# Kernel optimization log

Measured on AMD Instinct MI355X. Metric: run time of the kernel, lower is better.

The kernel has to match this reference:

```python
import jax, jax.numpy as jnp
import numpy as np
from jax import lax

VOCAB, EMB, HID, NCLS, BATCH, SEQ = 32000, 512, 512, 8, 64, 512


def setup_inputs() -> dict:
    key = jax.random.key(0)
    ks = jax.random.split(key, 12)
    s = 0.05
    return {
        "x": jax.random.randint(ks[0], (BATCH, SEQ), 0, VOCAB),
        "emb": jax.random.normal(ks[1], (VOCAB, EMB), jnp.float32) * s,
        "W_ih0": jax.random.normal(ks[2], (HID, EMB), jnp.float32) * s,
        "W_hh0": jax.random.normal(ks[3], (HID, HID), jnp.float32) * s,
        "b_ih0": jax.random.normal(ks[4], (HID,), jnp.float32) * s,
        "b_hh0": jax.random.normal(ks[5], (HID,), jnp.float32) * s,
        "W_ih1": jax.random.normal(ks[6], (HID, HID), jnp.float32) * s,
        "W_hh1": jax.random.normal(ks[7], (HID, HID), jnp.float32) * s,
        "b_ih1": jax.random.normal(ks[8], (HID,), jnp.float32) * s,
        "b_hh1": jax.random.normal(ks[9], (HID,), jnp.float32) * s,
        "fc_W": jax.random.normal(ks[10], (NCLS, HID), jnp.float32) * s,
        "fc_b": jax.random.normal(ks[11], (NCLS,), jnp.float32) * s,
    }


def _rnn_layer(inp, W_ih, W_hh, b_ih, b_hh):
    # inp: [B, S, F]; tanh RNN, batch_first. Precompute input projection once.
    pre = jnp.einsum('bsf,hf->bsh', inp, W_ih) + b_ih + b_hh  # [B,S,H]
    B = inp.shape[0]
    H = W_hh.shape[0]
    h0 = jnp.zeros((B, H), inp.dtype)

    def step(h, p_t):  # p_t: [B,H]
        h = jnp.tanh(p_t + h @ W_hh.T)
        return h, h

    hT, ys = lax.scan(step, h0, pre.transpose(1, 0, 2))  # scan over time
    return ys.transpose(1, 0, 2), hT  # outputs [B,S,H], last hidden [B,H]


def reference(x, emb, W_ih0, W_hh0, b_ih0, b_hh0, W_ih1, W_hh1, b_ih1, b_hh1, fc_W, fc_b):
    xe = emb[x]  # [B,S,E] embedding lookup
    out0, _ = _rnn_layer(xe, W_ih0, W_hh0, b_ih0, b_hh0)
    _, h1 = _rnn_layer(out0, W_ih1, W_hh1, b_ih1, b_hh1)  # hidden[-1]
    return h1 @ fc_W.T + fc_b  # [B, n_class]
```

## Files before the change

kernel.cpp:

```cpp
#include <hip/hip_runtime.h>
#include <stdint.h>


#define BB 64
#define SS 512
#define HH 512

typedef short bf16x8 __attribute__((ext_vector_type(8)));
typedef float f32x4 __attribute__((ext_vector_type(4)));
typedef int i32x4 __attribute__((ext_vector_type(4)));
typedef unsigned int u32;
typedef u32 u32x2 __attribute__((ext_vector_type(2)));

__device__ __forceinline__ unsigned short f2bf(float f) {
  uint32_t u = __builtin_bit_cast(uint32_t, f);
  u += 0x7FFFu + ((u >> 16) & 1u);
  return (unsigned short)(u >> 16);
}
__device__ __forceinline__ float bf2f(unsigned short h) {
  uint32_t u = ((uint32_t)h) << 16;
  return __builtin_bit_cast(float, u);
}
__device__ __forceinline__ int pack2(unsigned short a, unsigned short b) {
  return (int)(unsigned int)a | ((int)(unsigned int)b << 16);
}
__device__ __forceinline__ u32 hipack(u32 a, u32 b) {
  return (a >> 16) | (b & 0xFFFF0000u);
}
__device__ __forceinline__ u32 lopack(u32 a, u32 b) {
  return (a & 0xFFF8u) | ((b & 0xFFF8u) << 16);
}
__device__ __forceinline__ bool tag4(i32x4 v, u32 t) {
  u32 m = (((u32)v[0] ^ t) | ((u32)v[1] ^ t) | ((u32)v[2] ^ t) | ((u32)v[3] ^ t)) & 7u;
  return m == 0u;
}
__device__ __forceinline__ float fast_tanh(float v) {
  float a = __builtin_fabsf(v);
  float e = __expf(-2.0f * a);
  float t = (1.0f - e) / (1.0f + e);
  return __builtin_copysignf(t, v);
}

#define UC_LOAD4(dst, ptr) \
  asm volatile("global_load_dwordx4 %0, %1, off sc0 sc1" : "=v"(dst) : "v"(ptr))
#define UC_LOAD1(dst, ptr) \
  asm volatile("global_load_dword %0, %1, off sc0 sc1" : "=v"(dst) : "v"(ptr))
#define UC_STORE2(ptr, v) \
  asm volatile("global_store_dwordx2 %0, %1, off sc0 sc1" ::"v"(ptr), "v"(v) : "memory")

#define ISSUE8(a0, a1, a2, a3, a4, a5, a6, a7, base)  \
  do {                                                \
    UC_LOAD4(a0, (base) + 8 * gch + 0);               \
    UC_LOAD4(a1, (base) + 8 * gch + 4);               \
    UC_LOAD4(a2, (base) + 8 * gch + 128);             \
    UC_LOAD4(a3, (base) + 8 * gch + 132);             \
    UC_LOAD4(a4, (base) + 8 * gch + 256);             \
    UC_LOAD4(a5, (base) + 8 * gch + 260);             \
    UC_LOAD4(a6, (base) + 8 * gch + 384);             \
    UC_LOAD4(a7, (base) + 8 * gch + 388);             \
  } while (0)

#define TAGOK8(a0, a1, a2, a3, a4, a5, a6, a7, t)                         \
  (tag4(a0, t) && tag4(a1, t) && tag4(a2, t) && tag4(a3, t) &&            \
   tag4(a4, t) && tag4(a5, t) && tag4(a6, t) && tag4(a7, t))

#define STAGE_IN0(w0, w1, w2, w3, w4, w5, w6, w7)                          \
  do {                                                                     \
    i32x4 A;                                                               \
    A[0] = (int)hipack(w0[0], w0[1]); A[1] = (int)hipack(w0[2], w0[3]);    \
    A[2] = (int)hipack(w1[0], w1[1]); A[3] = (int)hipack(w1[2], w1[3]);    \
    *(i32x4*)(s_in0 + gr * 512 + (((gch + 0) ^ (gr & 7)) << 3)) = A;       \
    A[0] = (int)hipack(w2[0], w2[1]); A[1] = (int)hipack(w2[2], w2[3]);    \
    A[2] = (int)hipack(w3[0], w3[1]); A[3] = (int)hipack(w3[2], w3[3]);    \
    *(i32x4*)(s_in0 + gr * 512 + (((gch + 16) ^ (gr & 7)) << 3)) = A;      \
    A[0] = (int)hipack(w4[0], w4[1]); A[1] = (int)hipack(w4[2], w4[3]);    \
    A[2] = (int)hipack(w5[0], w5[1]); A[3] = (int)hipack(w5[2], w5[3]);    \
    *(i32x4*)(s_in0 + gr * 512 + (((gch + 32) ^ (gr & 7)) << 3)) = A;      \
    A[0] = (int)hipack(w6[0], w6[1]); A[1] = (int)hipack(w6[2], w6[3]);    \
    A[2] = (int)hipack(w7[0], w7[1]); A[3] = (int)hipack(w7[2], w7[3]);    \
    *(i32x4*)(s_in0 + gr * 512 + (((gch + 48) ^ (gr & 7)) << 3)) = A;      \
  } while (0)

#define STAGE_H(w0, w1, w2, w3, w4, w5, w6, w7)                            \
  do {                                                                     \
    i32x4 A, B;                                                            \
    A[0] = (int)hipack(w0[0], w0[1]); A[1] = (int)hipack(w0[2], w0[3]);    \
    A[2] = (int)hipack(w1[0], w1[1]); A[3] = (int)hipack(w1[2], w1[3]);    \
    B[0] = (int)lopack(w0[0], w0[1]); B[1] = (int)lopack(w0[2], w0[3]);    \
    B[2] = (int)lopack(w1[0], w1[1]); B[3] = (int)lopack(w1[2], w1[3]);    \
    *(i32x4*)(s_Hhi + gr * 512 + (((gch + 0) ^ (gr & 7)) << 3)) = A;       \
    *(i32x4*)(s_Hlo + gr * 512 + (((gch + 0) ^ (gr & 7)) << 3)) = B;       \
    A[0] = (int)hipack(w2[0], w2[1]); A[1] = (int)hipack(w2[2], w2[3]);    \
    A[2] = (int)hipack(w3[0], w3[1]); A[3] = (int)hipack(w3[2], w3[3]);    \
    B[0] = (int)lopack(w2[0], w2[1]); B[1] = (int)lopack(w2[2], w2[3]);    \
    B[2] = (int)lopack(w3[0], w3[1]); B[3] = (int)lopack(w3[2], w3[3]);    \
    *(i32x4*)(s_Hhi + gr * 512 + (((gch + 16) ^ (gr & 7)) << 3)) = A;      \
    *(i32x4*)(s_Hlo + gr * 512 + (((gch + 16) ^ (gr & 7)) << 3)) = B;      \
    A[0] = (int)hipack(w4[0], w4[1]); A[1] = (int)hipack(w4[2], w4[3]);    \
    A[2] = (int)hipack(w5[0], w5[1]); A[3] = (int)hipack(w5[2], w5[3]);    \
    B[0] = (int)lopack(w4[0], w4[1]); B[1] = (int)lopack(w4[2], w4[3]);    \
    B[2] = (int)lopack(w5[0], w5[1]); B[3] = (int)lopack(w5[2], w5[3]);    \
    *(i32x4*)(s_Hhi + gr * 512 + (((gch + 32) ^ (gr & 7)) << 3)) = A;      \
    *(i32x4*)(s_Hlo + gr * 512 + (((gch + 32) ^ (gr & 7)) << 3)) = B;      \
    A[0] = (int)hipack(w6[0], w6[1]); A[1] = (int)hipack(w6[2], w6[3]);    \
    A[2] = (int)hipack(w7[0], w7[1]); A[3] = (int)hipack(w7[2], w7[3]);    \
    B[0] = (int)lopack(w6[0], w6[1]); B[1] = (int)lopack(w6[2], w6[3]);    \
    B[2] = (int)lopack(w7[0], w7[1]); B[3] = (int)lopack(w7[2], w7[3]);    \
    *(i32x4*)(s_Hhi + gr * 512 + (((gch + 48) ^ (gr & 7)) << 3)) = A;      \
    *(i32x4*)(s_Hlo + gr * 512 + (((gch + 48) ^ (gr & 7)) << 3)) = B;      \
  } while (0)

__global__ __launch_bounds__(512, 1) void k_rnn(
    const int* __restrict__ x, const float* __restrict__ emb,
    const float* __restrict__ Wih0, const float* __restrict__ Whh0,
    const float* __restrict__ bih0, const float* __restrict__ bhh0,
    const float* __restrict__ Wih1, const float* __restrict__ Whh1,
    const float* __restrict__ bih1, const float* __restrict__ bhh1,
    u32* __restrict__ hsl) {
  const int tid = threadIdx.x;
  const int bid = blockIdx.x;
  const int layer = bid >> 5;
  const int lb = bid & 31;
  const int bg = lb >> 3;
  const int c = lb & 7;
  const int wid = tid >> 6;
  const int lane = tid & 63;
  const int kq = wid >> 1;
  const int nh = wid & 1;
  const int gt = tid & 255;
  const int gr = gt >> 4;
  const int gch = gt & 15;
  const int s_row = (wid & 3) * 4 + ((lane & 31) >> 3);
  const int s_pub = lane & 7;

  __shared__ __align__(16) unsigned short s_in0[16 * 512];
  __shared__ __align__(16) unsigned short s_Hhi[16 * 512];
  __shared__ __align__(16) unsigned short s_Hlo[16 * 512];
  __shared__ __align__(16) float s_part[4 * 16 * 64];

  const float* Wih = layer ? Wih1 : Wih0;
  const float* Whh = layer ? Whh1 : Whh0;
  const float* bi = layer ? bih1 : bih0;
  const float* bh = layer ? bhh1 : bhh0;

  bf16x8 wih[2][4], whhh[2][4], whhl[2][4];
  {
    const int r16 = lane & 15, kg = lane >> 4;
#pragma unroll
    for (int nt = 0; nt < 2; ++nt) {
#pragma unroll
      for (int kt = 0; kt < 4; ++kt) {
        int row = c * 64 + nh * 32 + nt * 16 + r16;
        int k0 = kq * 128 + kt * 32 + kg * 8;
        const float* p = Wih + row * 512 + k0;
        bf16x8 v;
#pragma unroll
        for (int j = 0; j < 8; ++j) v[j] = (short)f2bf(p[j]);
        wih[nt][kt] = v;
        const float* q = Whh + row * 512 + k0;
        bf16x8 vh, vl;
#pragma unroll
        for (int j = 0; j < 8; ++j) {
          float f = q[j];
          unsigned short h = f2bf(f);
          vh[j] = (short)h;
          vl[j] = (short)f2bf(f - bf2f(h));
        }
        whhh[nt][kt] = vh;
        whhl[nt][kt] = vl;
      }
    }
  }
  float biasv0, biasv1;
  {
    int na = (tid & 31) * 2;
    biasv0 = bi[c * 64 + na] + bh[c * 64 + na];
    biasv1 = bi[c * 64 + na + 1] + bh[c * 64 + na + 1];
  }

  float4 pf0, pf1, pf2, pf3, pf4, pf5, pf6, pf7;
  if (layer == 0 && wid < 4) {
    int rid = x[(bg * 16 + gr) * SS + 0];
    const float4* ep = (const float4*)(emb + (size_t)rid * 512);
    pf0 = ep[2 * gch + 0];  pf1 = ep[2 * gch + 1];
    pf2 = ep[2 * gch + 32]; pf3 = ep[2 * gch + 33];
    pf4 = ep[2 * gch + 64]; pf5 = ep[2 * gch + 65];
    pf6 = ep[2 * gch + 96]; pf7 = ep[2 * gch + 97];
  }

  for (int s = 1; s <= SS; ++s) {
    const u32 exp_h = (u32)((s - 1) & 7);

    if (wid < 4) {
      if (layer == 0) {
        {
          i32x4 v;
          v[0] = pack2(f2bf(pf0.x), f2bf(pf0.y));
          v[1] = pack2(f2bf(pf0.z), f2bf(pf0.w));
          v[2] = pack2(f2bf(pf1.x), f2bf(pf1.y));
          v[3] = pack2(f2bf(pf1.z), f2bf(pf1.w));
          *(i32x4*)(s_in0 + gr * 512 + (((gch + 0) ^ (gr & 7)) << 3)) = v;
          v[0] = pack2(f2bf(pf2.x), f2bf(pf2.y));
          v[1] = pack2(f2bf(pf2.z), f2bf(pf2.w));
          v[2] = pack2(f2bf(pf3.x), f2bf(pf3.y));
          v[3] = pack2(f2bf(pf3.z), f2bf(pf3.w));
          *(i32x4*)(s_in0 + gr * 512 + (((gch + 16) ^ (gr & 7)) << 3)) = v;
          v[0] = pack2(f2bf(pf4.x), f2bf(pf4.y));
          v[1] = pack2(f2bf(pf4.z), f2bf(pf4.w));
          v[2] = pack2(f2bf(pf5.x), f2bf(pf5.y));
          v[3] = pack2(f2bf(pf5.z), f2bf(pf5.w));
          *(i32x4*)(s_in0 + gr * 512 + (((gch + 32) ^ (gr & 7)) << 3)) = v;
          v[0] = pack2(f2bf(pf6.x), f2bf(pf6.y));
          v[1] = pack2(f2bf(pf6.z), f2bf(pf6.w));
          v[2] = pack2(f2bf(pf7.x), f2bf(pf7.y));
          v[3] = pack2(f2bf(pf7.z), f2bf(pf7.w));
          *(i32x4*)(s_in0 + gr * 512 + (((gch + 48) ^ (gr & 7)) << 3)) = v;
        }
        if (s < SS) {
          int rid = x[(bg * 16 + gr) * SS + s];
          const float4* ep = (const float4*)(emb + (size_t)rid * 512);
          pf0 = ep[2 * gch + 0];  pf1 = ep[2 * gch + 1];
          pf2 = ep[2 * gch + 32]; pf3 = ep[2 * gch + 33];
          pf4 = ep[2 * gch + 64]; pf5 = ep[2 * gch + 65];
          pf6 = ep[2 * gch + 96]; pf7 = ep[2 * gch + 97];
        }
      } else {
        const u32 exp_i = (u32)(s & 7);
        const u32* pib =
            hsl + (((size_t)(s & 3)) * 64 + bg * 16 + gr) * 512;
        {
          const u32* psent =
              hsl + (((size_t)(s & 3)) * 64 + bg * 16 + s_row) * 512 + s_pub * 64;
          u32 sw = 0;
          while (true) {
            UC_LOAD1(sw, psent);
            asm volatile("s_waitcnt vmcnt(0)" : "+v"(sw)::"memory");
            if (__all((sw & 7u) == exp_i)) break;
          }
        }
        i32x4 w0 = {0,0,0,0}, w1 = {0,0,0,0}, w2 = {0,0,0,0}, w3 = {0,0,0,0};
        i32x4 w4 = {0,0,0,0}, w5 = {0,0,0,0}, w6 = {0,0,0,0}, w7 = {0,0,0,0};
        while (true) {
          ISSUE8(w0, w1, w2, w3, w4, w5, w6, w7, pib);
          asm volatile("s_waitcnt vmcnt(0)"
                       : "+v"(w0), "+v"(w1), "+v"(w2), "+v"(w3), "+v"(w4),
                         "+v"(w5), "+v"(w6), "+v"(w7)::"memory");
          if (__all(TAGOK8(w0, w1, w2, w3, w4, w5, w6, w7, exp_i))) break;
        }
        STAGE_IN0(w0, w1, w2, w3, w4, w5, w6, w7);
      }
    } else {
      if (s > 1) {
        const u32* phb = hsl +
            (((size_t)layer * 4 + ((s - 1) & 3)) * 64 + bg * 16 + gr) * 512;
        {
          const u32* psent = hsl +
              (((size_t)layer * 4 + ((s - 1) & 3)) * 64 + bg * 16 + s_row) * 512 +
              s_pub * 64;
          const bool need_bp = (layer == 0) && (s > 4);
          const u32 exp_bp = (u32)((s - 4) & 7);
          const u32* pbp = hsl + ((size_t)(4 + ((s - 4) & 3)) * 64 + bg * 16) * 512 +
                           s_pub * 64;
          u32 sw = 0, bw = 0;
          while (true) {
            UC_LOAD1(sw, psent);
            if (need_bp) UC_LOAD1(bw, pbp);
            asm volatile("s_waitcnt vmcnt(0)" : "+v"(sw), "+v"(bw)::"memory");
            bool ok = ((sw & 7u) == exp_h) && (!need_bp || ((bw & 7u) == exp_bp));
            if (__all(ok)) break;
          }
        }
        i32x4 w0 = {0,0,0,0}, w1 = {0,0,0,0}, w2 = {0,0,0,0}, w3 = {0,0,0,0};
        i32x4 w4 = {0,0,0,0}, w5 = {0,0,0,0}, w6 = {0,0,0,0}, w7 = {0,0,0,0};
        while (true) {
          ISSUE8(w0, w1, w2, w3, w4, w5, w6, w7, phb);
          asm volatile("s_waitcnt vmcnt(0)"
                       : "+v"(w0), "+v"(w1), "+v"(w2), "+v"(w3), "+v"(w4),
                         "+v"(w5), "+v"(w6), "+v"(w7)::"memory");
          if (__all(TAGOK8(w0, w1, w2, w3, w4, w5, w6, w7, exp_h))) break;
        }
        STAGE_H(w0, w1, w2, w3, w4, w5, w6, w7);
      }
    }
    __syncthreads();

    f32x4 acc0 = {0.f, 0.f, 0.f, 0.f};
    f32x4 acc1 = {0.f, 0.f, 0.f, 0.f};
    {
      const int r16 = lane & 15, kg = lane >> 4;
#pragma unroll
      for (int kt = 0; kt < 4; ++kt) {
        int k8 = kq * 16 + kt * 4 + kg;
        bf16x8 ain = __builtin_bit_cast(
            bf16x8, *(const i32x4*)(s_in0 + r16 * 512 + ((k8 ^ (r16 & 7)) << 3)));
        acc0 = __builtin_amdgcn_mfma_f32_16x16x32_bf16(ain, wih[0][kt], acc0, 0, 0, 0);
        acc1 = __builtin_amdgcn_mfma_f32_16x16x32_bf16(ain, wih[1][kt], acc1, 0, 0, 0);
      }
      if (s > 1) {
#pragma unroll
        for (int kt = 0; kt < 4; ++kt) {
          int k8 = kq * 16 + kt * 4 + kg;
          bf16x8 ahi = __builtin_bit_cast(
              bf16x8, *(const i32x4*)(s_Hhi + r16 * 512 + ((k8 ^ (r16 & 7)) << 3)));
          bf16x8 alo = __builtin_bit_cast(
              bf16x8, *(const i32x4*)(s_Hlo + r16 * 512 + ((k8 ^ (r16 & 7)) << 3)));
          acc0 = __builtin_amdgcn_mfma_f32_16x16x32_bf16(ahi, whhh[0][kt], acc0, 0, 0, 0);
          acc0 = __builtin_amdgcn_mfma_f32_16x16x32_bf16(ahi, whhl[0][kt], acc0, 0, 0, 0);
          acc0 = __builtin_amdgcn_mfma_f32_16x16x32_bf16(alo, whhh[0][kt], acc0, 0, 0, 0);
          acc1 = __builtin_amdgcn_mfma_f32_16x16x32_bf16(ahi, whhh[1][kt], acc1, 0, 0, 0);
          acc1 = __builtin_amdgcn_mfma_f32_16x16x32_bf16(ahi, whhl[1][kt], acc1, 0, 0, 0);
          acc1 = __builtin_amdgcn_mfma_f32_16x16x32_bf16(alo, whhh[1][kt], acc1, 0, 0, 0);
        }
      }
#pragma unroll
      for (int j = 0; j < 4; ++j) {
        int m = kg * 4 + j;
        int xr = (m >> 2) & 3;
        int n0i = nh * 32 + 0 * 16 + r16;
        int n1i = nh * 32 + 1 * 16 + r16;
        s_part[kq * 1024 + m * 64 + (n0i ^ (xr << 4))] = acc0[j];
        s_part[kq * 1024 + m * 64 + (n1i ^ (xr << 4))] = acc1[j];
      }
    }
    __syncthreads();

    {
      int m = tid >> 5, na = (tid & 31) * 2;
      int xr = (m >> 2) & 3;
      float v0 = biasv0, v1 = biasv1;
#pragma unroll
      for (int q2 = 0; q2 < 4; ++q2) {
        const float2* sp =
            (const float2*)(s_part + q2 * 1024 + m * 64 + (na ^ (xr << 4)));
        float2 t = *sp;
        v0 += t.x;
        v1 += t.y;
      }
      v0 = fast_tanh(v0);
      v1 = fast_tanh(v1);
      unsigned short a0 = f2bf(v0), a1 = f2bf(v1);
      unsigned short b0 = f2bf(v0 - bf2f(a0)), b1 = f2bf(v1 - bf2f(a1));
      u32 tag = (u32)(s & 7);
      u32x2 wv;
      wv[0] = ((u32)a0 << 16) | ((u32)b0 & 0xFFF8u) | tag;
      wv[1] = ((u32)a1 << 16) | ((u32)b1 & 0xFFF8u) | tag;
      u32* dst = hsl + (((size_t)layer * 4 + (s & 3)) * 64 + bg * 16 + m) * 512 +
                 c * 64 + na;
      UC_STORE2(dst, wv);
    }
  }
}

__global__ void k_fc(const u32* __restrict__ h1w, const float* __restrict__ fcW,
                     const float* __restrict__ fcb, float* __restrict__ out) {
  int i = threadIdx.x;
  int b = i >> 3, cc = i & 7;
  float acc = fcb[cc];
  const u32* ph = h1w + b * 512;
  const float* pw = fcW + cc * 512;
  for (int k = 0; k < 512; k += 4) {
    int4 w4 = *(const int4*)(ph + k);
    float4 wv = *(const float4*)(pw + k);
    acc += (bf2f((unsigned short)((u32)w4.x >> 16)) +
            bf2f((unsigned short)((u32)w4.x & 0xFFF8u))) * wv.x;
    acc += (bf2f((unsigned short)((u32)w4.y >> 16)) +
            bf2f((unsigned short)((u32)w4.y & 0xFFF8u))) * wv.y;
    acc += (bf2f((unsigned short)((u32)w4.z >> 16)) +
            bf2f((unsigned short)((u32)w4.z & 0xFFF8u))) * wv.z;
    acc += (bf2f((unsigned short)((u32)w4.w >> 16)) +
            bf2f((unsigned short)((u32)w4.w & 0xFFF8u))) * wv.w;
  }
  out[b * 8 + cc] = acc;
}

extern "C" void kernel_launch(void* const* d_in, const int* in_sizes, int n_in,
                              void* d_out, int out_size, void* d_ws, size_t ws_size,
                              hipStream_t stream) {
  const int* x = (const int*)d_in[0];
  const float* emb = (const float*)d_in[1];
  const float* Wih0 = (const float*)d_in[2];
  const float* Whh0 = (const float*)d_in[3];
  const float* bih0 = (const float*)d_in[4];
  const float* bhh0 = (const float*)d_in[5];
  const float* Wih1 = (const float*)d_in[6];
  const float* Whh1 = (const float*)d_in[7];
  const float* bih1 = (const float*)d_in[8];
  const float* bhh1 = (const float*)d_in[9];
  const float* fcW = (const float*)d_in[10];
  const float* fcb = (const float*)d_in[11];

  u32* hsl = (u32*)d_ws;

  hipMemsetAsync(hsl, 0, (size_t)2 * 4 * 64 * 512 * 4, stream);
  hipLaunchKernelGGL(k_rnn, dim3(64), dim3(512), 0, stream, x, emb, Wih0, Whh0,
                     bih0, bhh0, Wih1, Whh1, bih1, bhh1, hsl);
  hipLaunchKernelGGL(k_fc, dim3(1), dim3(512), 0, stream,
                     hsl + (size_t)4 * 64 * 512, fcW, fcb, (float*)d_out);
}
```

Before: 1.881 ms.

## Drop sentinel pre-polls, move backpressure wait to input-prefetch waves, raise priority

Removes the single-word sentinel polling loops that ran before the full tagged 8-vector loads, so waves now spin directly on the tagged data loads. The layer-0 backpressure check on layer 1's progress moves out of the hidden-state waves and into the waves that prefetch embeddings, taking it off the recurrent critical path. The hidden-state waves also raise their scheduling priority while polling and staging. The tradeoff is heavier polling traffic, since each spin iteration now reissues eight 16-byte loads instead of one word.

```diff
diff --git a/kernel.cpp b/kernel.cpp
--- a/kernel.cpp
+++ b/kernel.cpp
@@ -130,8 +130,6 @@
   const int gt = tid & 255;
   const int gr = gt >> 4;
   const int gch = gt & 15;
-  const int s_row = (wid & 3) * 4 + ((lane & 31) >> 3);
-  const int s_pub = lane & 7;
 
   __shared__ __align__(16) unsigned short s_in0[16 * 512];
   __shared__ __align__(16) unsigned short s_Hhi[16 * 512];
@@ -224,22 +222,23 @@
           pf4 = ep[2 * gch + 64]; pf5 = ep[2 * gch + 65];
           pf6 = ep[2 * gch + 96]; pf7 = ep[2 * gch + 97];
         }
+        if (s > 4) {
+          const u32 exp_bp = (u32)((s - 4) & 7);
+          const u32* pbp = hsl + ((size_t)(4 + ((s - 4) & 3)) * 64 + bg * 16) * 512 +
+                           (gt < 8 ? gt * 64 : 0);
+          u32 bw = 0;
+          while (true) {
+            UC_LOAD1(bw, pbp);
+            asm volatile("s_waitcnt vmcnt(0)" : "+v"(bw)::"memory");
+            if (__all(gt >= 8 || ((bw & 7u) == exp_bp))) break;
+          }
+        }
       } else {
+        i32x4 w0 = {0,0,0,0}, w1 = {0,0,0,0}, w2 = {0,0,0,0}, w3 = {0,0,0,0};
+        i32x4 w4 = {0,0,0,0}, w5 = {0,0,0,0}, w6 = {0,0,0,0}, w7 = {0,0,0,0};
         const u32 exp_i = (u32)(s & 7);
         const u32* pib =
             hsl + (((size_t)(s & 3)) * 64 + bg * 16 + gr) * 512;
-        {
-          const u32* psent =
-              hsl + (((size_t)(s & 3)) * 64 + bg * 16 + s_row) * 512 + s_pub * 64;
-          u32 sw = 0;
-          while (true) {
-            UC_LOAD1(sw, psent);
-            asm volatile("s_waitcnt vmcnt(0)" : "+v"(sw)::"memory");
-            if (__all((sw & 7u) == exp_i)) break;
-          }
-        }
-        i32x4 w0 = {0,0,0,0}, w1 = {0,0,0,0}, w2 = {0,0,0,0}, w3 = {0,0,0,0};
-        i32x4 w4 = {0,0,0,0}, w5 = {0,0,0,0}, w6 = {0,0,0,0}, w7 = {0,0,0,0};
         while (true) {
           ISSUE8(w0, w1, w2, w3, w4, w5, w6, w7, pib);
           asm volatile("s_waitcnt vmcnt(0)"
@@ -251,27 +250,11 @@
       }
     } else {
       if (s > 1) {
+        __builtin_amdgcn_s_setprio(1);
+        i32x4 w0 = {0,0,0,0}, w1 = {0,0,0,0}, w2 = {0,0,0,0}, w3 = {0,0,0,0};
+        i32x4 w4 = {0,0,0,0}, w5 = {0,0,0,0}, w6 = {0,0,0,0}, w7 = {0,0,0,0};
         const u32* phb = hsl +
             (((size_t)layer * 4 + ((s - 1) & 3)) * 64 + bg * 16 + gr) * 512;
-        {
-          const u32* psent = hsl +
-              (((size_t)layer * 4 + ((s - 1) & 3)) * 64 + bg * 16 + s_row) * 512 +
-              s_pub * 64;
-          const bool need_bp = (layer == 0) && (s > 4);
-          const u32 exp_bp = (u32)((s - 4) & 7);
-          const u32* pbp = hsl + ((size_t)(4 + ((s - 4) & 3)) * 64 + bg * 16) * 512 +
-                           s_pub * 64;
-          u32 sw = 0, bw = 0;
-          while (true) {
-            UC_LOAD1(sw, psent);
-            if (need_bp) UC_LOAD1(bw, pbp);
-            asm volatile("s_waitcnt vmcnt(0)" : "+v"(sw), "+v"(bw)::"memory");
-            bool ok = ((sw & 7u) == exp_h) && (!need_bp || ((bw & 7u) == exp_bp));
-            if (__all(ok)) break;
-          }
-        }
-        i32x4 w0 = {0,0,0,0}, w1 = {0,0,0,0}, w2 = {0,0,0,0}, w3 = {0,0,0,0};
-        i32x4 w4 = {0,0,0,0}, w5 = {0,0,0,0}, w6 = {0,0,0,0}, w7 = {0,0,0,0};
         while (true) {
           ISSUE8(w0, w1, w2, w3, w4, w5, w6, w7, phb);
           asm volatile("s_waitcnt vmcnt(0)"
@@ -280,6 +263,7 @@
           if (__all(TAGOK8(w0, w1, w2, w3, w4, w5, w6, w7, exp_h))) break;
         }
         STAGE_H(w0, w1, w2, w3, w4, w5, w6, w7);
+        __builtin_amdgcn_s_setprio(0);
       }
     }
     __syncthreads();
```

New measurement: 1.727 ms, median of 2. 1.09x faster.
